# Kernel tuning notes

Hardware: AMD Instinct MI355X
Metric: run time of the kernel (lower is better)

Reference implementation:

```python
import jax, jax.numpy as jnp
import numpy as np

N_QUBITS = 20
N_TERMS = 4
BATCH = 16
DIM = 2 ** N_QUBITS


def _apply_two_qubit_gate(state, U, q0, q1):
    """Apply batched 4x4 unitary U (B,4,4) to qubit axes (q0,q1) of state (2,)*n+(B,)."""
    s = jnp.moveaxis(state, (q0, q1), (0, 1))
    rest = s.shape[2:-1]
    B = s.shape[-1]
    s = s.reshape(4, -1, B)  # (4, rest, B)
    out = jnp.einsum('bij,jrb->irb', U, s)
    out = out.reshape((2, 2) + rest + (B,))
    return jnp.moveaxis(out, (0, 1), (q0, q1))


def setup_inputs() -> dict:
    key = jax.random.key(0)
    k1, k2, k3, k4, k5 = jax.random.split(key, 5)
    H_real = jax.random.normal(k1, (N_TERMS, 4, 4), jnp.float32)
    H_imag = jax.random.normal(k2, (N_TERMS, 4, 4), jnp.float32)
    tevo = jax.random.uniform(k3, (N_TERMS, BATCH), jnp.float32)
    state_real = jax.random.normal(k4, (DIM, BATCH), jnp.float32)
    state_imag = jax.random.normal(k5, (DIM, BATCH), jnp.float32)
    nrm = jnp.sqrt(jnp.sum(state_real ** 2 + state_imag ** 2, axis=0, keepdims=True))
    return {'H_real': H_real, 'H_imag': H_imag, 'tevo': tevo,
            'state_real': state_real / nrm, 'state_imag': state_imag / nrm}


def reference(H_real, H_imag, tevo, state_real, state_imag):
    # Hermitian generators per term: H_k = (A + A^H)/2, A = H_real + i*H_imag  -> (K,4,4)
    A = H_real + 1j * H_imag
    H = 0.5 * (A + jnp.conj(jnp.swapaxes(A, -1, -2)))
    # Hamiltonian evolution U_k(t) = exp(-i H_k t) via eigendecomposition (HEvoPyQOperation)
    w, V = jnp.linalg.eigh(H)                       # w: (K,4) real, V: (K,4,4)
    phases = jnp.exp(-1j * w[:, None, :] * tevo[:, :, None])  # (K,B,4)
    U = jnp.einsum('kij,kbj,klj->kbil', V, phases, jnp.conj(V))  # (K,B,4,4)
    # statevector (2,)*n + (B,)
    state = (state_real + 1j * state_imag).reshape((2,) * N_QUBITS + (BATCH,))
    # AddPyQOperation: reduce(add, (op(state, values) for op in operations))
    out = jnp.zeros_like(state)
    for k in range(N_TERMS):
        out = out + _apply_two_qubit_gate(state, U[k], k, k + 1)
    out = out.reshape(DIM, BATCH)
    return jnp.stack([jnp.real(out), jnp.imag(out)])  # (2, DIM, B) real view of complex output
```

## Files before the change

kernel.cpp:

```cpp
#include <hip/hip_runtime.h>

#define NQ 20
#define DIMQ (1 << NQ)
#define NB 16
#define NT 4
#define RBITS 15
#define NCOL (1 << (RBITS + 4))

#define USTRIDE 36
#define UTOT (64 * USTRIDE)

__device__ __forceinline__ float dpp_swap1(float x) {
  int r = __builtin_amdgcn_mov_dpp(__builtin_bit_cast(int, x), 0xB1, 0xF, 0xF, true);
  return __builtin_bit_cast(float, r);
}

__device__ __forceinline__ void cfma(float2& o, const float2 u, const float2 s) {
  asm("v_pk_fma_f32 %0, %1, %2, %0 op_sel_hi:[0,1,1]\n\t"
      "v_pk_fma_f32 %0, %1, %2, %0 op_sel:[1,1,0] op_sel_hi:[1,0,1] neg_lo:[1,0,0]"
      : "+v"(o) : "v"(u), "v"(s));
}
__device__ __forceinline__ float2 cmul(const float2 u, const float2 s) {
  float2 o;
  asm("v_pk_mul_f32 %0, %1, %2 op_sel_hi:[0,1]\n\t"
      "v_pk_fma_f32 %0, %1, %2, %0 op_sel:[1,1,0] op_sel_hi:[1,0,1] neg_lo:[1,0,0]"
      : "=&v"(o) : "v"(u), "v"(s));
  return o;
}

__global__ __launch_bounds__(256) void compute_u_kernel(
    const float* __restrict__ Hre, const float* __restrict__ Him,
    const float* __restrict__ tevo, float* __restrict__ uout) {
  __shared__ float er_s[64][4][4];
  __shared__ float ei_s[64][4][4];

  const int tid  = threadIdx.x;
  const int task = tid >> 2;
  const int row  = tid & 3;
  const int k    = task >> 4;
  const int b    = task & 15;

  float Ar[4][4], Ai[4][4];
#pragma unroll
  for (int i = 0; i < 4; i++) {
#pragma unroll
    for (int j = 0; j < 4; j++) {
      Ar[i][j] = Hre[k * 16 + i * 4 + j];
      Ai[i][j] = Him[k * 16 + i * 4 + j];
    }
  }
  const float t = tevo[k * NB + b];
  const float ts = t * (1.0f / 16.0f);

  float Gr[4][4], Gi[4][4];
#pragma unroll
  for (int i = 0; i < 4; i++) {
#pragma unroll
    for (int j = 0; j < 4; j++) {
      const float hr = 0.5f * (Ar[i][j] + Ar[j][i]);
      const float hi = 0.5f * (Ai[i][j] - Ai[j][i]);
      Gr[i][j] = ts * hi;
      Gi[i][j] = -ts * hr;
    }
  }

  float Er[4], Ei[4], Tr[4], Ti[4];
#pragma unroll
  for (int j = 0; j < 4; j++) {
    Er[j] = (j == row) ? 1.0f : 0.0f;
    Ei[j] = 0.0f;
    Tr[j] = Er[j];
    Ti[j] = 0.0f;
  }
#pragma unroll
  for (int m = 1; m <= 8; m++) {
    const float inv = 1.0f / (float)m;
    float nr[4], ni[4];
#pragma unroll
    for (int j = 0; j < 4; j++) {
      float ar = 0.0f, ai = 0.0f;
#pragma unroll
      for (int p = 0; p < 4; p++) {
        ar += Tr[p] * Gr[p][j] - Ti[p] * Gi[p][j];
        ai += Tr[p] * Gi[p][j] + Ti[p] * Gr[p][j];
      }
      nr[j] = ar * inv;
      ni[j] = ai * inv;
    }
#pragma unroll
    for (int j = 0; j < 4; j++) {
      Tr[j] = nr[j]; Ti[j] = ni[j];
      Er[j] += nr[j]; Ei[j] += ni[j];
    }
  }

  for (int q = 0; q < 4; q++) {
    __syncthreads();
#pragma unroll
    for (int j = 0; j < 4; j++) {
      er_s[task][row][j] = Er[j];
      ei_s[task][row][j] = Ei[j];
    }
    __syncthreads();
    float nr[4], ni[4];
#pragma unroll
    for (int j = 0; j < 4; j++) {
      float ar = 0.0f, ai = 0.0f;
#pragma unroll
      for (int p = 0; p < 4; p++) {
        ar += Er[p] * er_s[task][p][j] - Ei[p] * ei_s[task][p][j];
        ai += Er[p] * ei_s[task][p][j] + Ei[p] * er_s[task][p][j];
      }
      nr[j] = ar; ni[j] = ai;
    }
#pragma unroll
    for (int j = 0; j < 4; j++) { Er[j] = nr[j]; Ei[j] = ni[j]; }
  }

  const int ubase = (k * 16 + b) * USTRIDE;
#pragma unroll
  for (int j = 0; j < 4; j++) {
    uout[ubase + (row * 4 + j) * 2]     = Er[j];
    uout[ubase + (row * 4 + j) * 2 + 1] = Ei[j];
  }
}

__global__ __launch_bounds__(256, 4) void apply_gates_kernel(
    const float* __restrict__ sre, const float* __restrict__ sim,
    const float* __restrict__ u, float* __restrict__ out) {
  __shared__ __align__(16) float ul[UTOT];
  const int tid   = threadIdx.x;
  const int half  = tid & 1;
  const int col   = blockIdx.x * 128 + (tid >> 1);
  const int b     = (tid >> 1) & 15;
  const int gbase = half << 4;

  float2 s[16];
#pragma unroll
  for (int q = 0; q < 16; q++) {
    const int off = col + ((gbase + q) << 19);
    s[q].x = sre[off];
    s[q].y = sim[off];
  }

  const int l = tid & 63;
  {
    const float4* u4 = (const float4*)u;
    float4* ul4 = (float4*)ul;
#pragma unroll
    for (int t = 0; t < 9; t++) ul4[l + 64 * t] = u4[l + 64 * t];
  }

  float2 o[16];

  {
    const float* ub0 = &ul[b * USTRIDE];
    const int h4 = half * 4;
#pragma unroll
    for (int b3 = 0; b3 < 2; b3++) {
      const float4 vo = *(const float4*)(ub0 + (half * 2 + b3) * 8 + h4);
      const float4 vc = *(const float4*)(ub0 + ((half ^ 1) * 2 + b3) * 8 + h4);
      const float2 vo0 = make_float2(vo.x, vo.y), vo1 = make_float2(vo.z, vo.w);
      const float2 vc0 = make_float2(vc.x, vc.y), vc1 = make_float2(vc.z, vc.w);
#pragma unroll
      for (int ll = 0; ll < 8; ll++) {
        const int gq = b3 * 8 + ll;
        o[gq] = cmul(vo0, s[ll]);
        cfma(o[gq], vo1, s[8 + ll]);
        float2 p = cmul(vc0, s[ll]);
        cfma(p, vc1, s[8 + ll]);
        o[gq].x += dpp_swap1(p.x);
        o[gq].y += dpp_swap1(p.y);
      }
    }
  }

#pragma unroll
  for (int k = 1; k < 4; k++) {
    const int sh = 3 - k;
    const float* ub = &ul[(k * 16 + b) * USTRIDE];
#pragma unroll
    for (int i = 0; i < 4; i++) {
      const float4 v0 = *(const float4*)(ub + i * 8);
      const float4 v1 = *(const float4*)(ub + i * 8 + 4);
      const float2 u0 = make_float2(v0.x, v0.y), u1 = make_float2(v0.z, v0.w);
      const float2 u2 = make_float2(v1.x, v1.y), u3 = make_float2(v1.z, v1.w);
#pragma unroll
      for (int qq = 0; qq < 4; qq++) {
        const int low  = qq & ((1 << sh) - 1);
        const int high = (qq >> sh) << (sh + 2);
        const int gb   = high | low;
        const int gq   = gb | (i << sh);
        cfma(o[gq], u0, s[gb]);
        cfma(o[gq], u1, s[gb | (1 << sh)]);
        cfma(o[gq], u2, s[gb | (2 << sh)]);
        cfma(o[gq], u3, s[gb | (3 << sh)]);
      }
    }
  }

#pragma unroll
  for (int q = 0; q < 16; q++) {
    const int off = col + ((gbase + q) << 19);
    __builtin_nontemporal_store(o[q].x, out + off);
    __builtin_nontemporal_store(o[q].y, out + off + (1 << 24));
  }
}

extern "C" void kernel_launch(void* const* d_in, const int* in_sizes, int n_in,
                              void* d_out, int out_size, void* d_ws, size_t ws_size,
                              hipStream_t stream) {
  const float* Hre  = (const float*)d_in[0];
  const float* Him  = (const float*)d_in[1];
  const float* tevo = (const float*)d_in[2];
  const float* sre  = (const float*)d_in[3];
  const float* sim  = (const float*)d_in[4];
  float* out = (float*)d_out;
  float* uws = (float*)d_ws;

  compute_u_kernel<<<1, 256, 0, stream>>>(Hre, Him, tevo, uws);
  apply_gates_kernel<<<NCOL / 128, 256, 0, stream>>>(sre, sim, uws, out);
}
```

Baseline: 53.21 us.

## Stage state tile through LDS with async global loads and split qubit work by wave

The gate-apply kernel now pulls a 64-column tile of the state (all 32 top-qubit slices, real and imaginary) into shared memory with global_load_lds 16-byte async copies. Each wave then owns 8 of the 32 top-qubit slices. The q0/q1 cross terms are read from shared memory instead of being exchanged through DPP lane swaps. The aim is wider, more coalesced loads and fewer registers per thread, with twice as many blocks. The cost is 16KB of extra LDS per block, a barrier, and redundant LDS reads for the cross-wave terms.

New measurement: 51.14 us. 1.04x faster.

```diff
diff --git a/kernel.cpp b/kernel.cpp
--- a/kernel.cpp
+++ b/kernel.cpp
@@ -10,11 +10,6 @@
 #define USTRIDE 36
 #define UTOT (64 * USTRIDE)
 
-__device__ __forceinline__ float dpp_swap1(float x) {
-  int r = __builtin_amdgcn_mov_dpp(__builtin_bit_cast(int, x), 0xB1, 0xF, 0xF, true);
-  return __builtin_bit_cast(float, r);
-}
-
 __device__ __forceinline__ void cfma(float2& o, const float2 u, const float2 s) {
   asm("v_pk_fma_f32 %0, %1, %2, %0 op_sel_hi:[0,1,1]\n\t"
       "v_pk_fma_f32 %0, %1, %2, %0 op_sel:[1,1,0] op_sel_hi:[1,0,1] neg_lo:[1,0,0]"
@@ -129,56 +124,42 @@
     const float* __restrict__ sre, const float* __restrict__ sim,
     const float* __restrict__ u, float* __restrict__ out) {
   __shared__ __align__(16) float ul[UTOT];
-  const int tid   = threadIdx.x;
-  const int half  = tid & 1;
-  const int col   = blockIdx.x * 128 + (tid >> 1);
-  const int b     = (tid >> 1) & 15;
-  const int gbase = half << 4;
-
-  float2 s[16];
-#pragma unroll
-  for (int q = 0; q < 16; q++) {
-    const int off = col + ((gbase + q) << 19);
-    s[q].x = sre[off];
-    s[q].y = sim[off];
-  }
-
-  const int l = tid & 63;
-  {
-    const float4* u4 = (const float4*)u;
-    float4* ul4 = (float4*)ul;
-#pragma unroll
-    for (int t = 0; t < 9; t++) ul4[l + 64 * t] = u4[l + 64 * t];
-  }
-
-  float2 o[16];
-
-  {
-    const float* ub0 = &ul[b * USTRIDE];
-    const int h4 = half * 4;
-#pragma unroll
-    for (int b3 = 0; b3 < 2; b3++) {
-      const float4 vo = *(const float4*)(ub0 + (half * 2 + b3) * 8 + h4);
-      const float4 vc = *(const float4*)(ub0 + ((half ^ 1) * 2 + b3) * 8 + h4);
-      const float2 vo0 = make_float2(vo.x, vo.y), vo1 = make_float2(vo.z, vo.w);
-      const float2 vc0 = make_float2(vc.x, vc.y), vc1 = make_float2(vc.z, vc.w);
-#pragma unroll
-      for (int ll = 0; ll < 8; ll++) {
-        const int gq = b3 * 8 + ll;
-        o[gq] = cmul(vo0, s[ll]);
-        cfma(o[gq], vo1, s[8 + ll]);
-        float2 p = cmul(vc0, s[ll]);
-        cfma(p, vc1, s[8 + ll]);
-        o[gq].x += dpp_swap1(p.x);
-        o[gq].y += dpp_swap1(p.y);
-      }
-    }
-  }
-
-#pragma unroll
-  for (int k = 1; k < 4; k++) {
-    const int sh = 3 - k;
-    const float* ub = &ul[(k * 16 + b) * USTRIDE];
+  __shared__ __align__(16) float st[64 * 64];
+  const int tid = threadIdx.x;
+  const int w   = tid >> 6;
+  const int l   = tid & 63;
+  const int c0  = blockIdx.x * 64;
+  const int b   = l & 15;
+  const int q0  = w & 1;
+
+#pragma unroll
+  for (int t = 0; t < 4; t++) {
+    const int p  = w * 4 + t;
+    const int pl = p * 4 + (l >> 4);
+    const int g  = pl & 31;
+    const float* src = (pl < 32 ? sre : sim) + (g << 19) + c0 + (l & 15) * 4;
+    float* dst = st + p * 256;
+    __builtin_amdgcn_global_load_lds(
+        (const __attribute__((address_space(1))) float*)(const void*)src,
+        (__attribute__((address_space(3))) float*)(void*)dst, 16, 0, 0);
+  }
+
+#pragma unroll
+  for (int q = 0; q < 9; q++) ul[tid + q * 256] = u[tid + q * 256];
+
+  __syncthreads();
+
+  float2 s[8];
+#pragma unroll
+  for (int m = 0; m < 8; m++) {
+    s[m].x = st[(w * 8 + m) * 64 + l];
+    s[m].y = st[(32 + w * 8 + m) * 64 + l];
+  }
+
+  float2 o[8];
+
+  {
+    const float* ub = &ul[(3 * 16 + b) * USTRIDE];
 #pragma unroll
     for (int i = 0; i < 4; i++) {
       const float4 v0 = *(const float4*)(ub + i * 8);
@@ -186,24 +167,90 @@
       const float2 u0 = make_float2(v0.x, v0.y), u1 = make_float2(v0.z, v0.w);
       const float2 u2 = make_float2(v1.x, v1.y), u3 = make_float2(v1.z, v1.w);
 #pragma unroll
-      for (int qq = 0; qq < 4; qq++) {
-        const int low  = qq & ((1 << sh) - 1);
-        const int high = (qq >> sh) << (sh + 2);
-        const int gb   = high | low;
-        const int gq   = gb | (i << sh);
-        cfma(o[gq], u0, s[gb]);
-        cfma(o[gq], u1, s[gb | (1 << sh)]);
-        cfma(o[gq], u2, s[gb | (2 << sh)]);
-        cfma(o[gq], u3, s[gb | (3 << sh)]);
-      }
-    }
-  }
-
-#pragma unroll
-  for (int q = 0; q < 16; q++) {
-    const int off = col + ((gbase + q) << 19);
-    __builtin_nontemporal_store(o[q].x, out + off);
-    __builtin_nontemporal_store(o[q].y, out + off + (1 << 24));
+      for (int h = 0; h < 2; h++) {
+        const int om = h * 4 + i;
+        o[om] = cmul(u0, s[h * 4 + 0]);
+        cfma(o[om], u1, s[h * 4 + 1]);
+        cfma(o[om], u2, s[h * 4 + 2]);
+        cfma(o[om], u3, s[h * 4 + 3]);
+      }
+    }
+  }
+
+  {
+    const float* ub = &ul[(2 * 16 + b) * USTRIDE];
+#pragma unroll
+    for (int i = 0; i < 4; i++) {
+      const float4 v0 = *(const float4*)(ub + i * 8);
+      const float4 v1 = *(const float4*)(ub + i * 8 + 4);
+      const float2 u0 = make_float2(v0.x, v0.y), u1 = make_float2(v0.z, v0.w);
+      const float2 u2 = make_float2(v1.x, v1.y), u3 = make_float2(v1.z, v1.w);
+#pragma unroll
+      for (int l0 = 0; l0 < 2; l0++) {
+        const int om = i * 2 + l0;
+        cfma(o[om], u0, s[l0]);
+        cfma(o[om], u1, s[2 + l0]);
+        cfma(o[om], u2, s[4 + l0]);
+        cfma(o[om], u3, s[6 + l0]);
+      }
+    }
+  }
+
+  {
+    float2 p[8];
+    const int pq = w ^ 1;
+#pragma unroll
+    for (int m = 0; m < 8; m++) {
+      p[m].x = st[(pq * 8 + m) * 64 + l];
+      p[m].y = st[(32 + pq * 8 + m) * 64 + l];
+    }
+    const float* ub1 = &ul[(1 * 16 + b) * USTRIDE];
+#pragma unroll
+    for (int mh = 0; mh < 2; mh++) {
+      const int i = q0 * 2 + mh;
+      const float* row = ub1 + i * 8;
+#pragma unroll
+      for (int j2 = 0; j2 < 2; j2++) {
+        const float2 uo = *(const float2*)(row + (q0 * 2 + j2) * 2);
+        const float2 up = *(const float2*)(row + ((q0 ^ 1) * 2 + j2) * 2);
+#pragma unroll
+        for (int ml = 0; ml < 4; ml++) {
+          const int om = mh * 4 + ml;
+          cfma(o[om], uo, s[j2 * 4 + ml]);
+          cfma(o[om], up, p[j2 * 4 + ml]);
+        }
+      }
+    }
+    const float* ub0 = &ul[b * USTRIDE];
+    const float2 u01 = *(const float2*)(ub0 + (w * 4 + (w ^ 1)) * 2);
+#pragma unroll
+    for (int m = 0; m < 8; m++) cfma(o[m], u01, p[m]);
+  }
+
+  {
+    const float* ub0 = &ul[b * USTRIDE];
+    const float2 u00 = *(const float2*)(ub0 + (w * 4 + w) * 2);
+#pragma unroll
+    for (int m = 0; m < 8; m++) cfma(o[m], u00, s[m]);
+#pragma unroll
+    for (int d = 2; d < 4; d++) {
+      const int jq = w ^ d;
+      const float2 uj = *(const float2*)(ub0 + (w * 4 + jq) * 2);
+#pragma unroll
+      for (int m = 0; m < 8; m++) {
+        float2 t;
+        t.x = st[(jq * 8 + m) * 64 + l];
+        t.y = st[(32 + jq * 8 + m) * 64 + l];
+        cfma(o[m], uj, t);
+      }
+    }
+  }
+
+#pragma unroll
+  for (int m = 0; m < 8; m++) {
+    const int off = c0 + l + ((w * 8 + m) << 19);
+    __builtin_nontemporal_store(o[m].x, out + off);
+    __builtin_nontemporal_store(o[m].y, out + off + (1 << 24));
   }
 }
 
@@ -219,5 +266,5 @@
   float* uws = (float*)d_ws;
 
   compute_u_kernel<<<1, 256, 0, stream>>>(Hre, Him, tevo, uws);
-  apply_gates_kernel<<<NCOL / 128, 256, 0, stream>>>(sre, sim, uws, out);
-}
+  apply_gates_kernel<<<NCOL / 64, 256, 0, stream>>>(sre, sim, uws, out);
+}
```
